# Kernel tuning notes

Hardware: AMD Instinct MI355X
Metric: run time of the kernel (lower is better)

Reference implementation:

```python
import jax, jax.numpy as jnp
import numpy as np

ATTENTION_HEAD = 16
EXPANSION_LENGTH = 300
TEXT_EMBEDDING_DIM = 768
LN_EPS = 1e-3  # keras LayerNormalization default epsilon


def setup_inputs() -> dict:
    key = jax.random.key(0)
    ks = jax.random.split(key, 8)
    B, L, D = 8, 2048, TEXT_EMBEDDING_DIM
    H = ATTENTION_HEAD
    E = EXPANSION_LENGTH
    dh = D // H
    glorot = lambda k, shape, fan_in, fan_out: jax.random.uniform(
        k, shape, jnp.float32,
        -jnp.sqrt(6.0 / (fan_in + fan_out)), jnp.sqrt(6.0 / (fan_in + fan_out)))
    return {
        "q": jax.random.normal(ks[0], (B, 1, L, D), jnp.float32),
        "k": jax.random.normal(ks[1], (B, 1, L, D), jnp.float32),
        "v": jax.random.normal(ks[2], (B, 1, L, D), jnp.float32),
        "Wq": glorot(ks[3], (D, D), D, D),
        "bq": jnp.zeros((D,), jnp.float32),
        "Wv": glorot(ks[4], (D, D), D, D),
        "bv": jnp.zeros((D,), jnp.float32),
        "memory": glorot(ks[5], (E, H, dh), E, dh),
        "gamma": jnp.ones((D,), jnp.float32),
        "beta": jnp.zeros((D,), jnp.float32),
    }


def reference(q, k, v, Wq, bq, Wv, bv, memory, gamma, beta):
    B, _, L, D = q.shape
    H = ATTENTION_HEAD
    dh = D // H
    # Dense projections (v is unused by the original module)
    Q_ = q @ Wq + bq                      # (B,1,L,D)
    V_ = k @ Wv + bv                      # (B,1,L,D)
    Q = Q_.reshape(B, L, H, dh)
    V = V_.reshape(B, L, H, dh)
    # memory-query scores, ReLU instead of softmax
    eij = jax.nn.relu(jnp.einsum('ehd,blhd->belh', memory, Q))  # (B,E,L,H)
    out1 = jnp.einsum('belh,blhd->behd', eij, V)                # (B,E,H,dh)
    out2 = jnp.einsum('behd,belh->blhd', out1, eij)             # (B,L,H,dh)
    x = out2.reshape(B, 1, L, D)
    mean = jnp.mean(x, axis=-1, keepdims=True)
    var = jnp.var(x, axis=-1, keepdims=True)
    return (x - mean) * jax.lax.rsqrt(var + LN_EPS) * gamma + beta
```

## Files before the change

### kernel.cpp

```cpp
#include <hip/hip_runtime.h>
#include <hip/hip_bf16.h>
#include <stdint.h>

#define B_   8
#define L_   2048
#define D_   768
#define H_   16
#define DH   48
#define E_   300
#define EP   320
#define KP   64
#define ACH  8
#define N1T  (128 * DH * EP)
#define NT_  24

typedef __bf16 bf16;
typedef __bf16 bf16x8 __attribute__((ext_vector_type(8)));
typedef __bf16 bf16x4 __attribute__((ext_vector_type(4)));
typedef float  f32x4  __attribute__((ext_vector_type(4)));

typedef const __attribute__((address_space(1))) uint32_t guint;
typedef __attribute__((address_space(3))) uint32_t luint;

__device__ __forceinline__ f32x4 mfma16(bf16x8 a, bf16x8 b, f32x4 c) {
  return __builtin_amdgcn_mfma_f32_16x16x32_bf16(a, b, c, 0, 0, 0);
}

__global__ __launch_bounds__(256) void k_cast(const float* __restrict__ q,
                                              const float* __restrict__ k,
                                              bf16* __restrict__ qc,
                                              bf16* __restrict__ kc) {
  const float* src = blockIdx.y ? k : q;
  bf16* dst = blockIdx.y ? kc : qc;
  const int n8 = B_ * L_ * D_ / 8;
  for (int i = blockIdx.x * 256 + threadIdx.x; i < n8; i += gridDim.x * 256) {
    float4 f0 = *(const float4*)(src + (size_t)i * 8);
    float4 f1 = *(const float4*)(src + (size_t)i * 8 + 4);
    bf16x8 v;
    v[0] = (bf16)f0.x; v[1] = (bf16)f0.y; v[2] = (bf16)f0.z; v[3] = (bf16)f0.w;
    v[4] = (bf16)f1.x; v[5] = (bf16)f1.y; v[6] = (bf16)f1.z; v[7] = (bf16)f1.w;
    *(bf16x8*)(dst + (size_t)i * 8) = v;
  }
}

__global__ __launch_bounds__(256) void k_prep(
    const float* __restrict__ Wq, const float* __restrict__ Wv,
    const float* __restrict__ M, bf16* __restrict__ WqT,
    bf16* __restrict__ WvT, bf16* __restrict__ MP) {
  int bid = blockIdx.x;
  if (bid < 4608) {
    int which = bid / 2304;
    int idx = (bid % 2304) * 256 + threadIdx.x;
    int n = idx / D_, k = idx % D_;
    const float* W = which ? Wv : Wq;
    bf16* WT = which ? WvT : WqT;
    WT[n * D_ + k] = (bf16)W[k * D_ + n];
  } else {
    int idx = (bid - 4608) * 256 + threadIdx.x;
    int h = idx / (EP * KP);
    int r = idx % (EP * KP);
    int e = r / KP, d = r % KP;
    float v = (e < E_ && d < DH) ? M[(e * H_ + h) * DH + d] : 0.f;
    MP[idx] = (bf16)v;
  }
}

__global__ __launch_bounds__(256, 3) void k_gemm(
    const bf16* __restrict__ A0, const bf16* __restrict__ A1,
    const bf16* __restrict__ WT0, const bf16* __restrict__ WT1,
    const float* __restrict__ b0, const float* __restrict__ b1,
    bf16* __restrict__ outQ, bf16* __restrict__ outVT) {
  __shared__ bf16 As[3][128 * 32];
  __shared__ bf16 Bs[3][128 * 32];
  const int tid = threadIdx.x, lane = tid & 63, w = tid >> 6;
  const int wr = w >> 1, wc = w & 1;
  const int lr = lane & 15, lq = lane >> 4;
  const int bid = blockIdx.x;
  const int j = (bid & 7) * 96 + (bid >> 3);
  const int n0 = (j % 6) * 128, m0 = (j / 6) * 128;
  const int mode = blockIdx.y;
  const bf16* A = mode ? A1 : A0;
  const bf16* WT = mode ? WT1 : WT0;
  const float* bias = mode ? b1 : b0;

  auto stage = [&](int buf, int k0) {
#pragma unroll
    for (int p = 0; p < 2; ++p) {
      int idx = tid + p * 256;
      int row = idx >> 2, ct = idx & 3;
      int gc = ct ^ ((row >> 1) & 3);
      const bf16* src = A + (size_t)(m0 + row) * D_ + k0 + gc * 8;
      __builtin_amdgcn_global_load_lds((guint*)src,
          (luint*)&As[buf][(p * 256 + w * 64) * 8], 16, 0, 0);
    }
#pragma unroll
    for (int p = 0; p < 2; ++p) {
      int idx = tid + p * 256;
      int row = idx >> 2, ct = idx & 3;
      int gc = ct ^ ((row >> 1) & 3);
      const bf16* src = WT + (size_t)(n0 + row) * D_ + k0 + gc * 8;
      __builtin_amdgcn_global_load_lds((guint*)src,
          (luint*)&Bs[buf][(p * 256 + w * 64) * 8], 16, 0, 0);
    }
  };

  f32x4 acc[4][4] = {};

  stage(0, 0);
  stage(1, 32);

#pragma unroll
  for (int t = 0; t < NT_; ++t) {
    const int cur = t % 3;
    if (t + 1 < NT_) asm volatile("s_waitcnt vmcnt(4) lgkmcnt(0)" ::: "memory");
    else             asm volatile("s_waitcnt vmcnt(0) lgkmcnt(0)" ::: "memory");
    __builtin_amdgcn_s_barrier();
    __builtin_amdgcn_sched_barrier(0);
    if (t + 2 < NT_) stage((t + 2) % 3, (t + 2) * 32);

    bf16x8 af[4], bfr[4];
#pragma unroll
    for (int mi = 0; mi < 4; ++mi) {
      int row = wr * 64 + mi * 16 + lr;
      af[mi] = *(const bf16x8*)&As[cur][row * 32 + ((lq ^ ((row >> 1) & 3)) * 8)];
    }
#pragma unroll
    for (int ni = 0; ni < 4; ++ni) {
      int row = wc * 64 + ni * 16 + lr;
      bfr[ni] = *(const bf16x8*)&Bs[cur][row * 32 + ((lq ^ ((row >> 1) & 3)) * 8)];
    }
    __builtin_amdgcn_s_setprio(1);
#pragma unroll
    for (int mi = 0; mi < 4; ++mi)
#pragma unroll
      for (int ni = 0; ni < 4; ++ni)
        acc[mi][ni] = mfma16(af[mi], bfr[ni], acc[mi][ni]);
    __builtin_amdgcn_s_setprio(0);
  }

  float bs[4];
#pragma unroll
  for (int ni = 0; ni < 4; ++ni) bs[ni] = bias[n0 + wc * 64 + ni * 16 + lr];

  if (mode == 0) {
#pragma unroll
    for (int mi = 0; mi < 4; ++mi)
#pragma unroll
      for (int ni = 0; ni < 4; ++ni) {
        int m = m0 + wr * 64 + mi * 16 + lq * 4;
        int n = n0 + wc * 64 + ni * 16 + lr;
#pragma unroll
        for (int r = 0; r < 4; ++r)
          outQ[(size_t)(m + r) * D_ + n] = (bf16)(acc[mi][ni][r] + bs[ni]);
      }
  } else {
#pragma unroll
    for (int mi = 0; mi < 4; ++mi)
#pragma unroll
      for (int ni = 0; ni < 4; ++ni) {
        int mb = m0 + wr * 64 + mi * 16 + lq * 4;
        int n = n0 + wc * 64 + ni * 16 + lr;
        int bhd = (mb >> 11) * H_ + n / DH;
        int d = n % DH;
        int l = mb & (L_ - 1);
        bf16x4 v;
#pragma unroll
        for (int r = 0; r < 4; ++r) v[r] = (bf16)(acc[mi][ni][r] + bs[ni]);
        *(bf16x4*)&outVT[((size_t)bhd * DH + d) * L_ + l] = v;
      }
  }
}

__global__ __launch_bounds__(256) void k_phaseA(
    const bf16* __restrict__ Qb, const bf16* __restrict__ VT,
    const bf16* __restrict__ MP, bf16* __restrict__ O1P) {
  __shared__ bf16 Qs[2][32 * 88];
  __shared__ bf16 Vs[2][48 * 40];
  __shared__ bf16 Ss[EP * 40];
  const int tid = threadIdx.x, lane = tid & 63, w = tid >> 6;
  const int lr = lane & 15, lq = lane >> 4;
  const int bid = blockIdx.x;
  const int jj = (bid & 7) * 128 + (bid >> 3);
  const int bh = jj >> 3, b = bh >> 4, h = bh & 15;
  const int ach = jj & 7;
  const int lbase = ach * (L_ / ACH);

  bf16x8 mf[5][2];
#pragma unroll
  for (int mi = 0; mi < 5; ++mi)
#pragma unroll
    for (int kh = 0; kh < 2; ++kh)
      mf[mi][kh] = *(const bf16x8*)&MP[(size_t)(h * EP + w * 80 + mi * 16 + lr) * KP + kh * 32 + lq * 8];

  if (tid < 128) {
    int buf = tid >> 6, t = tid & 63;
    uint4 z = {0, 0, 0, 0};
    *(uint4*)&Qs[buf][(t >> 1) * 88 + 48 + (t & 1) * 8] = z;
  }

  auto loadQ = [&](int idx, int l0) {
    return *(const bf16x8*)&Qb[(size_t)(b * L_ + l0 + idx / 6) * D_ + h * DH + (idx % 6) * 8];
  };
  auto loadV = [&](int j, int l0) {
    return *(const bf16x8*)&VT[((size_t)bh * DH + (j >> 2)) * L_ + l0 + (j & 3) * 8];
  };

  bf16x8 rA, rB;
  {
    int l0 = lbase;
    rA = (tid < 192) ? loadQ(tid, l0) : loadV(tid - 192, l0);
    if (tid < 128) rB = loadV(tid + 64, l0);
  }

  f32x4 acc[5][3] = {};

  for (int it = 0; it < L_ / ACH / 32; ++it) {
    const int cur = it & 1;
    if (tid < 192) *(bf16x8*)&Qs[cur][(tid / 6) * 88 + (tid % 6) * 8] = rA;
    else           *(bf16x8*)&Vs[cur][((tid - 192) >> 2) * 40 + ((tid - 192) & 3) * 8] = rA;
    if (tid < 128) *(bf16x8*)&Vs[cur][((tid + 64) >> 2) * 40 + ((tid + 64) & 3) * 8] = rB;
    __syncthreads();
    if (it + 1 < L_ / ACH / 32) {
      int l0 = lbase + (it + 1) * 32;
      rA = (tid < 192) ? loadQ(tid, l0) : loadV(tid - 192, l0);
      if (tid < 128) rB = loadV(tid + 64, l0);
    }
    bf16x8 qf[2][2];
#pragma unroll
    for (int ni = 0; ni < 2; ++ni)
#pragma unroll
      for (int kh = 0; kh < 2; ++kh)
        qf[ni][kh] = *(const bf16x8*)&Qs[cur][(ni * 16 + lr) * 88 + kh * 32 + lq * 8];
    __builtin_amdgcn_s_setprio(1);
#pragma unroll
    for (int mi = 0; mi < 5; ++mi)
#pragma unroll
      for (int ni = 0; ni < 2; ++ni) {
        f32x4 s = {0.f, 0.f, 0.f, 0.f};
        s = mfma16(mf[mi][0], qf[ni][0], s);
        s = mfma16(mf[mi][1], qf[ni][1], s);
#pragma unroll
        for (int r = 0; r < 4; ++r)
          Ss[(w * 80 + mi * 16 + lq * 4 + r) * 40 + ni * 16 + lr] =
              (bf16)(s[r] > 0.f ? s[r] : 0.f);
      }
    __builtin_amdgcn_s_setprio(0);
    bf16x8 sf[5], vf[3];
#pragma unroll
    for (int mi = 0; mi < 5; ++mi)
      sf[mi] = *(const bf16x8*)&Ss[(w * 80 + mi * 16 + lr) * 40 + lq * 8];
#pragma unroll
    for (int ni = 0; ni < 3; ++ni)
      vf[ni] = *(const bf16x8*)&Vs[cur][(ni * 16 + lr) * 40 + lq * 8];
    __builtin_amdgcn_s_setprio(1);
#pragma unroll
    for (int mi = 0; mi < 5; ++mi)
#pragma unroll
      for (int ni = 0; ni < 3; ++ni)
        acc[mi][ni] = mfma16(sf[mi], vf[ni], acc[mi][ni]);
    __builtin_amdgcn_s_setprio(0);
  }
  bf16* dst = O1P + (size_t)(ach * 128 + bh) * DH * EP;
#pragma unroll
  for (int mi = 0; mi < 5; ++mi)
#pragma unroll
    for (int ni = 0; ni < 3; ++ni) {
      int e = w * 80 + mi * 16 + lq * 4;
      int d = ni * 16 + lr;
      bf16x4 v;
#pragma unroll
      for (int r = 0; r < 4; ++r) v[r] = (bf16)acc[mi][ni][r];
      *(bf16x4*)&dst[(size_t)d * EP + e] = v;
    }
}

__global__ __launch_bounds__(256) void k_red(const bf16* __restrict__ O1P,
                                             bf16* __restrict__ O1T) {
  int i8 = blockIdx.x * 256 + threadIdx.x;
  if (i8 >= N1T / 8) return;
  float s[8] = {};
#pragma unroll
  for (int c = 0; c < ACH; ++c) {
    bf16x8 v = *(const bf16x8*)&O1P[(size_t)c * N1T + (size_t)i8 * 8];
#pragma unroll
    for (int j = 0; j < 8; ++j) s[j] += (float)v[j];
  }
  bf16x8 o;
#pragma unroll
  for (int j = 0; j < 8; ++j) o[j] = (bf16)s[j];
  *(bf16x8*)&O1T[(size_t)i8 * 8] = o;
}

__global__ __launch_bounds__(256, 4) void k_phaseB(
    const bf16* __restrict__ Qb, const bf16* __restrict__ MP,
    const bf16* __restrict__ O1T, bf16* __restrict__ X) {
  __shared__ bf16 Qs[64 * 88];
  __shared__ bf16 STs[64 * 76];
  __shared__ bf16 O1s[2][48 * 76];
  const int tid = threadIdx.x, lane = tid & 63, w = tid >> 6;
  const int lr = lane & 15, lq = lane >> 4;
  const int bid = blockIdx.x;
  const int jj = (bid & 7) * 512 + (bid >> 3);
  const int bh = jj >> 5, b = bh >> 4, h = bh & 15;
  const int l0 = (jj & 31) * 64;

  bf16x8 mfB[5][2];
#pragma unroll
  for (int c = 0; c < 5; ++c)
#pragma unroll
    for (int kh = 0; kh < 2; ++kh)
      mfB[c][kh] = *(const bf16x8*)&MP[(size_t)(h * EP + c * 64 + w * 16 + lr) * KP + kh * 32 + lq * 8];

  for (int idx = tid; idx < 512; idx += 256) {
    if (idx < 384) {
      int row = idx / 6, c = idx % 6;
      *(bf16x8*)&Qs[row * 88 + c * 8] =
          *(const bf16x8*)&Qb[(size_t)(b * L_ + l0 + row) * D_ + h * DH + c * 8];
    } else {
      int j = idx - 384;
      uint4 z = {0, 0, 0, 0};
      *(uint4*)&Qs[(j >> 1) * 88 + 48 + (j & 1) * 8] = z;
    }
  }
  for (int idx = tid; idx < 384; idx += 256)
    *(bf16x8*)&O1s[0][(idx >> 3) * 76 + (idx & 7) * 8] =
        *(const bf16x8*)&O1T[((size_t)bh * DH + (idx >> 3)) * EP + (idx & 7) * 8];
  __syncthreads();

  f32x4 acc[3] = {};
#pragma unroll
  for (int c = 0; c < 5; ++c) {
    bf16x8 r0, r1;
    if (c < 4) {
      r0 = *(const bf16x8*)&O1T[((size_t)bh * DH + (tid >> 3)) * EP + (c + 1) * 64 + (tid & 7) * 8];
      if (tid < 128) {
        int i2 = tid + 256;
        r1 = *(const bf16x8*)&O1T[((size_t)bh * DH + (i2 >> 3)) * EP + (c + 1) * 64 + (i2 & 7) * 8];
      }
    }
    __builtin_amdgcn_s_setprio(1);
#pragma unroll
    for (int mi = 0; mi < 4; ++mi) {
      bf16x8 qa0 = *(const bf16x8*)&Qs[(mi * 16 + lr) * 88 + lq * 8];
      bf16x8 qa1 = *(const bf16x8*)&Qs[(mi * 16 + lr) * 88 + 32 + lq * 8];
      f32x4 s = {0.f, 0.f, 0.f, 0.f};
      s = mfma16(qa0, mfB[c][0], s);
      s = mfma16(qa1, mfB[c][1], s);
#pragma unroll
      for (int r = 0; r < 4; ++r)
        STs[(mi * 16 + lq * 4 + r) * 76 + w * 16 + lr] =
            (bf16)(s[r] > 0.f ? s[r] : 0.f);
    }
    __builtin_amdgcn_s_setprio(0);
    __syncthreads();
    __builtin_amdgcn_s_setprio(1);
#pragma unroll
    for (int ks = 0; ks < 2; ++ks) {
      bf16x8 sf = *(const bf16x8*)&STs[(w * 16 + lr) * 76 + ks * 32 + lq * 8];
#pragma unroll
      for (int ni = 0; ni < 3; ++ni) {
        bf16x8 of = *(const bf16x8*)&O1s[c & 1][(ni * 16 + lr) * 76 + ks * 32 + lq * 8];
        acc[ni] = mfma16(sf, of, acc[ni]);
      }
    }
    __builtin_amdgcn_s_setprio(0);
    if (c < 4) {
      *(bf16x8*)&O1s[(c + 1) & 1][(tid >> 3) * 76 + (tid & 7) * 8] = r0;
      if (tid < 128) {
        int i2 = tid + 256;
        *(bf16x8*)&O1s[(c + 1) & 1][(i2 >> 3) * 76 + (i2 & 7) * 8] = r1;
      }
    }
    __syncthreads();
  }
#pragma unroll
  for (int ni = 0; ni < 3; ++ni)
#pragma unroll
    for (int r = 0; r < 4; ++r)
      X[(size_t)(b * L_ + l0 + w * 16 + lq * 4 + r) * D_ + h * DH + ni * 16 + lr] =
          (bf16)acc[ni][r];
}

__global__ __launch_bounds__(256) void k_ln(
    const bf16* __restrict__ X, const float* __restrict__ gamma,
    const float* __restrict__ beta, float* __restrict__ out) {
  const int lane = threadIdx.x & 63;
  const int row = blockIdx.x * 4 + (threadIdx.x >> 6);
  const bf16* x = X + (size_t)row * D_;
  float v[12];
#pragma unroll
  for (int c = 0; c < 3; ++c) {
    bf16x4 ch = *(const bf16x4*)(x + lane * 12 + c * 4);
#pragma unroll
    for (int j = 0; j < 4; ++j) v[c * 4 + j] = (float)ch[j];
  }
  float s = 0.f, q = 0.f;
#pragma unroll
  for (int j = 0; j < 12; ++j) { s += v[j]; q += v[j] * v[j]; }
#pragma unroll
  for (int off = 32; off > 0; off >>= 1) {
    s += __shfl_xor(s, off);
    q += __shfl_xor(q, off);
  }
  float mean = s * (1.f / 768.f);
  float var = q * (1.f / 768.f) - mean * mean;
  float inv = rsqrtf(var + 1e-3f);
  float* o = out + (size_t)row * D_;
#pragma unroll
  for (int c = 0; c < 3; ++c) {
    float4 g = *(const float4*)(gamma + lane * 12 + c * 4);
    float4 bt = *(const float4*)(beta + lane * 12 + c * 4);
    float4 r;
    r.x = (v[c * 4 + 0] - mean) * inv * g.x + bt.x;
    r.y = (v[c * 4 + 1] - mean) * inv * g.y + bt.y;
    r.z = (v[c * 4 + 2] - mean) * inv * g.z + bt.z;
    r.w = (v[c * 4 + 3] - mean) * inv * g.w + bt.w;
    *(float4*)(o + lane * 12 + c * 4) = r;
  }
}

extern "C" void kernel_launch(void* const* d_in, const int* in_sizes, int n_in,
                              void* d_out, int out_size, void* d_ws, size_t ws_size,
                              hipStream_t stream) {
  (void)in_sizes; (void)n_in; (void)out_size; (void)ws_size;
  const float* q_in = (const float*)d_in[0];
  const float* k_in = (const float*)d_in[1];
  const float* Wq   = (const float*)d_in[3];
  const float* bq   = (const float*)d_in[4];
  const float* Wv   = (const float*)d_in[5];
  const float* bv   = (const float*)d_in[6];
  const float* mem  = (const float*)d_in[7];
  const float* gam  = (const float*)d_in[8];
  const float* bet  = (const float*)d_in[9];
  float* out = (float*)d_out;

  char* ws = (char*)d_ws;
  size_t off = 0;
  auto alloc = [&](size_t bytes) {
    char* p = ws + off;
    off += (bytes + 255) & ~(size_t)255;
    return p;
  };
  bf16*  WqT = (bf16*)alloc((size_t)D_ * D_ * 2);
  bf16*  WvT = (bf16*)alloc((size_t)D_ * D_ * 2);
  bf16*  MP  = (bf16*)alloc((size_t)H_ * EP * KP * 2);
  bf16*  Qb  = (bf16*)alloc((size_t)B_ * L_ * D_ * 2);
  bf16*  VT  = (bf16*)alloc((size_t)B_ * H_ * DH * L_ * 2);
  bf16*  O1T = (bf16*)alloc((size_t)N1T * 2);
  const size_t castHalf  = ((size_t)B_ * L_ * D_ * 2 + 256) & ~(size_t)255;
  const size_t castBytes = 2 * castHalf;
  const size_t o1pBytes  = (size_t)ACH * N1T * 2;
  size_t bigBytes = castBytes > o1pBytes ? castBytes : o1pBytes;
  char*  big = alloc(bigBytes);
  bf16*  qc  = (bf16*)big;
  bf16*  kc  = (bf16*)(big + castHalf);
  bf16*  O1P = (bf16*)big;
  bf16*  Xb  = (bf16*)big;

  k_cast<<<dim3(2048, 2), 256, 0, stream>>>(q_in, k_in, qc, kc);
  k_prep<<<5888, 256, 0, stream>>>(Wq, Wv, mem, WqT, WvT, MP);
  k_gemm<<<dim3(768, 2), 256, 0, stream>>>(qc, kc, WqT, WvT, bq, bv, Qb, VT);
  k_phaseA<<<1024, 256, 0, stream>>>(Qb, VT, MP, O1P);
  k_red<<<(N1T / 8 + 255) / 256, 256, 0, stream>>>(O1P, O1T);
  k_phaseB<<<4096, 256, 0, stream>>>(Qb, MP, O1T, Xb);
  k_ln<<<(B_ * L_) / 4, 256, 0, stream>>>(Xb, gam, bet, out);
}
```

Baseline: 191.9 us.

## Fuse fp32-to-bf16 cast of q/k into GEMM A-tile loading

Removes the separate cast kernel and has the projection GEMM load fp32 activations into registers, convert them to bf16, and write them to swizzled LDS, using a register-staged three-deep prefetch. This drops a full bf16 write and re-read of q and k plus one kernel launch. In exchange, GEMM A-tile traffic doubles (fp32), the loads no longer go directly to LDS, register pressure rises, and the pipeline's wait counts are restructured.

```diff
diff --git a/kernel.cpp b/kernel.cpp
--- a/kernel.cpp
+++ b/kernel.cpp
@@ -24,23 +24,6 @@
 
 __device__ __forceinline__ f32x4 mfma16(bf16x8 a, bf16x8 b, f32x4 c) {
   return __builtin_amdgcn_mfma_f32_16x16x32_bf16(a, b, c, 0, 0, 0);
-}
-
-__global__ __launch_bounds__(256) void k_cast(const float* __restrict__ q,
-                                              const float* __restrict__ k,
-                                              bf16* __restrict__ qc,
-                                              bf16* __restrict__ kc) {
-  const float* src = blockIdx.y ? k : q;
-  bf16* dst = blockIdx.y ? kc : qc;
-  const int n8 = B_ * L_ * D_ / 8;
-  for (int i = blockIdx.x * 256 + threadIdx.x; i < n8; i += gridDim.x * 256) {
-    float4 f0 = *(const float4*)(src + (size_t)i * 8);
-    float4 f1 = *(const float4*)(src + (size_t)i * 8 + 4);
-    bf16x8 v;
-    v[0] = (bf16)f0.x; v[1] = (bf16)f0.y; v[2] = (bf16)f0.z; v[3] = (bf16)f0.w;
-    v[4] = (bf16)f1.x; v[5] = (bf16)f1.y; v[6] = (bf16)f1.z; v[7] = (bf16)f1.w;
-    *(bf16x8*)(dst + (size_t)i * 8) = v;
-  }
 }
 
 __global__ __launch_bounds__(256) void k_prep(
@@ -66,7 +49,7 @@
 }
 
 __global__ __launch_bounds__(256, 3) void k_gemm(
-    const bf16* __restrict__ A0, const bf16* __restrict__ A1,
+    const float* __restrict__ A0, const float* __restrict__ A1,
     const bf16* __restrict__ WT0, const bf16* __restrict__ WT1,
     const float* __restrict__ b0, const float* __restrict__ b1,
     bf16* __restrict__ outQ, bf16* __restrict__ outVT) {
@@ -79,20 +62,15 @@
   const int j = (bid & 7) * 96 + (bid >> 3);
   const int n0 = (j % 6) * 128, m0 = (j / 6) * 128;
   const int mode = blockIdx.y;
-  const bf16* A = mode ? A1 : A0;
+  const float* A = mode ? A1 : A0;
   const bf16* WT = mode ? WT1 : WT0;
   const float* bias = mode ? b1 : b0;
 
-  auto stage = [&](int buf, int k0) {
-#pragma unroll
-    for (int p = 0; p < 2; ++p) {
-      int idx = tid + p * 256;
-      int row = idx >> 2, ct = idx & 3;
-      int gc = ct ^ ((row >> 1) & 3);
-      const bf16* src = A + (size_t)(m0 + row) * D_ + k0 + gc * 8;
-      __builtin_amdgcn_global_load_lds((guint*)src,
-          (luint*)&As[buf][(p * 256 + w * 64) * 8], 16, 0, 0);
-    }
+  const int arow = tid >> 2, ac = tid & 3;
+  const int aslot = ac ^ ((arow >> 1) & 3);
+  const float* aSrc = A + (size_t)(m0 + arow) * D_ + ac * 8;
+
+  auto stageB = [&](int buf, int k0) {
 #pragma unroll
     for (int p = 0; p < 2; ++p) {
       int idx = tid + p * 256;
@@ -105,18 +83,48 @@
   };
 
   f32x4 acc[4][4] = {};
-
-  stage(0, 0);
-  stage(1, 32);
+  float4 ar[3][4];
+
+#define LOADA(G, T)                                                \
+  { const float* s0_ = aSrc + (T) * 32;                            \
+    ar[G][0] = *(const float4*)s0_;                                \
+    ar[G][1] = *(const float4*)(s0_ + 4);                          \
+    const float* s1_ = s0_ + (size_t)64 * D_;                      \
+    ar[G][2] = *(const float4*)s1_;                                \
+    ar[G][3] = *(const float4*)(s1_ + 4); }
+#define COMMITA(G, BUF)                                            \
+  { bf16x8 v_;                                                     \
+    v_[0]=(bf16)ar[G][0].x; v_[1]=(bf16)ar[G][0].y;                \
+    v_[2]=(bf16)ar[G][0].z; v_[3]=(bf16)ar[G][0].w;                \
+    v_[4]=(bf16)ar[G][1].x; v_[5]=(bf16)ar[G][1].y;                \
+    v_[6]=(bf16)ar[G][1].z; v_[7]=(bf16)ar[G][1].w;                \
+    *(bf16x8*)&As[BUF][arow * 32 + aslot * 8] = v_;                \
+    v_[0]=(bf16)ar[G][2].x; v_[1]=(bf16)ar[G][2].y;                \
+    v_[2]=(bf16)ar[G][2].z; v_[3]=(bf16)ar[G][2].w;                \
+    v_[4]=(bf16)ar[G][3].x; v_[5]=(bf16)ar[G][3].y;                \
+    v_[6]=(bf16)ar[G][3].z; v_[7]=(bf16)ar[G][3].w;                \
+    *(bf16x8*)&As[BUF][(arow + 64) * 32 + aslot * 8] = v_; }
+#define SBAR __builtin_amdgcn_sched_barrier(0)
+
+  LOADA(0, 0);  SBAR;
+  stageB(0, 0); SBAR;
+  LOADA(1, 1);  SBAR;
+  stageB(1, 32); SBAR;
+  LOADA(2, 2);  SBAR;
+  COMMITA(0, 0);
 
 #pragma unroll
   for (int t = 0; t < NT_; ++t) {
     const int cur = t % 3;
-    if (t + 1 < NT_) asm volatile("s_waitcnt vmcnt(4) lgkmcnt(0)" ::: "memory");
-    else             asm volatile("s_waitcnt vmcnt(0) lgkmcnt(0)" ::: "memory");
+    if (t + 1 < NT_) { COMMITA((t + 1) % 3, (t + 1) % 3); }
+    else { asm volatile("s_waitcnt vmcnt(0)" ::: "memory"); }
+    asm volatile("s_waitcnt lgkmcnt(0)" ::: "memory");
     __builtin_amdgcn_s_barrier();
-    __builtin_amdgcn_sched_barrier(0);
-    if (t + 2 < NT_) stage((t + 2) % 3, (t + 2) * 32);
+    SBAR;
+    if (t + 2 < NT_) stageB((t + 2) % 3, (t + 2) * 32);
+    SBAR;
+    if (t + 3 < NT_) LOADA(t % 3, t + 3);
+    SBAR;
 
     bf16x8 af[4], bfr[4];
 #pragma unroll
@@ -137,6 +145,9 @@
         acc[mi][ni] = mfma16(af[mi], bfr[ni], acc[mi][ni]);
     __builtin_amdgcn_s_setprio(0);
   }
+#undef LOADA
+#undef COMMITA
+#undef SBAR
 
   float bs[4];
 #pragma unroll
@@ -447,19 +458,14 @@
   bf16*  Qb  = (bf16*)alloc((size_t)B_ * L_ * D_ * 2);
   bf16*  VT  = (bf16*)alloc((size_t)B_ * H_ * DH * L_ * 2);
   bf16*  O1T = (bf16*)alloc((size_t)N1T * 2);
-  const size_t castHalf  = ((size_t)B_ * L_ * D_ * 2 + 256) & ~(size_t)255;
-  const size_t castBytes = 2 * castHalf;
-  const size_t o1pBytes  = (size_t)ACH * N1T * 2;
-  size_t bigBytes = castBytes > o1pBytes ? castBytes : o1pBytes;
-  char*  big = alloc(bigBytes);
-  bf16*  qc  = (bf16*)big;
-  bf16*  kc  = (bf16*)(big + castHalf);
+  const size_t o1pBytes = (size_t)ACH * N1T * 2;
+  const size_t xbBytes  = (size_t)B_ * L_ * D_ * 2;
+  char*  big = alloc(o1pBytes > xbBytes ? o1pBytes : xbBytes);
   bf16*  O1P = (bf16*)big;
   bf16*  Xb  = (bf16*)big;
 
-  k_cast<<<dim3(2048, 2), 256, 0, stream>>>(q_in, k_in, qc, kc);
   k_prep<<<5888, 256, 0, stream>>>(Wq, Wv, mem, WqT, WvT, MP);
-  k_gemm<<<dim3(768, 2), 256, 0, stream>>>(qc, kc, WqT, WvT, bq, bv, Qb, VT);
+  k_gemm<<<dim3(768, 2), 256, 0, stream>>>(q_in, k_in, WqT, WvT, bq, bv, Qb, VT);
   k_phaseA<<<1024, 256, 0, stream>>>(Qb, VT, MP, O1P);
   k_red<<<(N1T / 8 + 255) / 256, 256, 0, stream>>>(O1P, O1T);
   k_phaseB<<<4096, 256, 0, stream>>>(Qb, MP, O1T, Xb);
```

After: 188.0 us. 2.0% less time.

## Merge cast and prep kernels; restructure phaseB to per-wave rows without barriers

Applied to the files above, without the earlier changes.

The separate cast and weight/memory prep kernels are merged into one launch with a flat block index, removing one kernel launch. In phaseB each wave now owns its own 16 rows of Q and computes all 64 score columns itself, so the score tile is written and read only by the same wave and the block-level syncs go away. O1T fragments are read straight from global memory instead of being double-buffered through LDS, and memory fragments are loaded per chunk instead of being kept in registers. This removes barriers and LDS traffic, at the cost of more global/L2 reads and redundant memory-fragment loads across waves.

```diff
diff --git a/kernel.cpp b/kernel.cpp
--- a/kernel.cpp
+++ b/kernel.cpp
@@ -26,37 +26,32 @@
   return __builtin_amdgcn_mfma_f32_16x16x32_bf16(a, b, c, 0, 0, 0);
 }
 
-__global__ __launch_bounds__(256) void k_cast(const float* __restrict__ q,
-                                              const float* __restrict__ k,
-                                              bf16* __restrict__ qc,
-                                              bf16* __restrict__ kc) {
-  const float* src = blockIdx.y ? k : q;
-  bf16* dst = blockIdx.y ? kc : qc;
-  const int n8 = B_ * L_ * D_ / 8;
-  for (int i = blockIdx.x * 256 + threadIdx.x; i < n8; i += gridDim.x * 256) {
+__global__ __launch_bounds__(256) void k_prep2(
+    const float* __restrict__ q, const float* __restrict__ k,
+    const float* __restrict__ Wq, const float* __restrict__ Wv,
+    const float* __restrict__ M, bf16* __restrict__ qc,
+    bf16* __restrict__ kc, bf16* __restrict__ WqT,
+    bf16* __restrict__ WvT, bf16* __restrict__ MP) {
+  int bid = blockIdx.x;
+  if (bid < 12288) {
+    const float* src = bid < 6144 ? q : k;
+    bf16* dst = bid < 6144 ? qc : kc;
+    int i = (bid < 6144 ? bid : bid - 6144) * 256 + threadIdx.x;
     float4 f0 = *(const float4*)(src + (size_t)i * 8);
     float4 f1 = *(const float4*)(src + (size_t)i * 8 + 4);
     bf16x8 v;
     v[0] = (bf16)f0.x; v[1] = (bf16)f0.y; v[2] = (bf16)f0.z; v[3] = (bf16)f0.w;
     v[4] = (bf16)f1.x; v[5] = (bf16)f1.y; v[6] = (bf16)f1.z; v[7] = (bf16)f1.w;
     *(bf16x8*)(dst + (size_t)i * 8) = v;
-  }
-}
-
-__global__ __launch_bounds__(256) void k_prep(
-    const float* __restrict__ Wq, const float* __restrict__ Wv,
-    const float* __restrict__ M, bf16* __restrict__ WqT,
-    bf16* __restrict__ WvT, bf16* __restrict__ MP) {
-  int bid = blockIdx.x;
-  if (bid < 4608) {
-    int which = bid / 2304;
-    int idx = (bid % 2304) * 256 + threadIdx.x;
-    int n = idx / D_, k = idx % D_;
+  } else if (bid < 16896) {
+    int which = (bid - 12288) / 2304;
+    int idx = ((bid - 12288) % 2304) * 256 + threadIdx.x;
+    int n = idx / D_, kk = idx % D_;
     const float* W = which ? Wv : Wq;
     bf16* WT = which ? WvT : WqT;
-    WT[n * D_ + k] = (bf16)W[k * D_ + n];
+    WT[n * D_ + kk] = (bf16)W[kk * D_ + n];
   } else {
-    int idx = (bid - 4608) * 256 + threadIdx.x;
+    int idx = (bid - 16896) * 256 + threadIdx.x;
     int h = idx / (EP * KP);
     int r = idx % (EP * KP);
     int e = r / KP, d = r % KP;
@@ -105,7 +100,6 @@
   };
 
   f32x4 acc[4][4] = {};
-
   stage(0, 0);
   stage(1, 32);
 
@@ -295,21 +289,13 @@
     const bf16* __restrict__ Qb, const bf16* __restrict__ MP,
     const bf16* __restrict__ O1T, bf16* __restrict__ X) {
   __shared__ bf16 Qs[64 * 88];
-  __shared__ bf16 STs[64 * 76];
-  __shared__ bf16 O1s[2][48 * 76];
+  __shared__ bf16 STs[64 * 72];
   const int tid = threadIdx.x, lane = tid & 63, w = tid >> 6;
   const int lr = lane & 15, lq = lane >> 4;
   const int bid = blockIdx.x;
   const int jj = (bid & 7) * 512 + (bid >> 3);
   const int bh = jj >> 5, b = bh >> 4, h = bh & 15;
   const int l0 = (jj & 31) * 64;
-
-  bf16x8 mfB[5][2];
-#pragma unroll
-  for (int c = 0; c < 5; ++c)
-#pragma unroll
-    for (int kh = 0; kh < 2; ++kh)
-      mfB[c][kh] = *(const bf16x8*)&MP[(size_t)(h * EP + c * 64 + w * 16 + lr) * KP + kh * 32 + lq * 8];
 
   for (int idx = tid; idx < 512; idx += 256) {
     if (idx < 384) {
@@ -322,56 +308,42 @@
       *(uint4*)&Qs[(j >> 1) * 88 + 48 + (j & 1) * 8] = z;
     }
   }
-  for (int idx = tid; idx < 384; idx += 256)
-    *(bf16x8*)&O1s[0][(idx >> 3) * 76 + (idx & 7) * 8] =
-        *(const bf16x8*)&O1T[((size_t)bh * DH + (idx >> 3)) * EP + (idx & 7) * 8];
   __syncthreads();
 
+  bf16x8 qa[2];
+  qa[0] = *(const bf16x8*)&Qs[(w * 16 + lr) * 88 + lq * 8];
+  qa[1] = *(const bf16x8*)&Qs[(w * 16 + lr) * 88 + 32 + lq * 8];
+
   f32x4 acc[3] = {};
 #pragma unroll
   for (int c = 0; c < 5; ++c) {
-    bf16x8 r0, r1;
-    if (c < 4) {
-      r0 = *(const bf16x8*)&O1T[((size_t)bh * DH + (tid >> 3)) * EP + (c + 1) * 64 + (tid & 7) * 8];
-      if (tid < 128) {
-        int i2 = tid + 256;
-        r1 = *(const bf16x8*)&O1T[((size_t)bh * DH + (i2 >> 3)) * EP + (c + 1) * 64 + (i2 & 7) * 8];
-      }
-    }
+    bf16x8 mf[4][2];
+#pragma unroll
+    for (int et = 0; et < 4; ++et)
+#pragma unroll
+      for (int kh = 0; kh < 2; ++kh)
+        mf[et][kh] = *(const bf16x8*)&MP[(size_t)(h * EP + c * 64 + et * 16 + lr) * KP + kh * 32 + lq * 8];
     __builtin_amdgcn_s_setprio(1);
 #pragma unroll
-    for (int mi = 0; mi < 4; ++mi) {
-      bf16x8 qa0 = *(const bf16x8*)&Qs[(mi * 16 + lr) * 88 + lq * 8];
-      bf16x8 qa1 = *(const bf16x8*)&Qs[(mi * 16 + lr) * 88 + 32 + lq * 8];
+    for (int et = 0; et < 4; ++et) {
       f32x4 s = {0.f, 0.f, 0.f, 0.f};
-      s = mfma16(qa0, mfB[c][0], s);
-      s = mfma16(qa1, mfB[c][1], s);
+      s = mfma16(qa[0], mf[et][0], s);
+      s = mfma16(qa[1], mf[et][1], s);
 #pragma unroll
       for (int r = 0; r < 4; ++r)
-        STs[(mi * 16 + lq * 4 + r) * 76 + w * 16 + lr] =
+        STs[(w * 16 + lq * 4 + r) * 72 + et * 16 + lr] =
             (bf16)(s[r] > 0.f ? s[r] : 0.f);
     }
     __builtin_amdgcn_s_setprio(0);
-    __syncthreads();
-    __builtin_amdgcn_s_setprio(1);
 #pragma unroll
     for (int ks = 0; ks < 2; ++ks) {
-      bf16x8 sf = *(const bf16x8*)&STs[(w * 16 + lr) * 76 + ks * 32 + lq * 8];
+      bf16x8 sf = *(const bf16x8*)&STs[(w * 16 + lr) * 72 + ks * 32 + lq * 8];
 #pragma unroll
       for (int ni = 0; ni < 3; ++ni) {
-        bf16x8 of = *(const bf16x8*)&O1s[c & 1][(ni * 16 + lr) * 76 + ks * 32 + lq * 8];
+        bf16x8 of = *(const bf16x8*)&O1T[((size_t)bh * DH + ni * 16 + lr) * EP + c * 64 + ks * 32 + lq * 8];
         acc[ni] = mfma16(sf, of, acc[ni]);
       }
     }
-    __builtin_amdgcn_s_setprio(0);
-    if (c < 4) {
-      *(bf16x8*)&O1s[(c + 1) & 1][(tid >> 3) * 76 + (tid & 7) * 8] = r0;
-      if (tid < 128) {
-        int i2 = tid + 256;
-        *(bf16x8*)&O1s[(c + 1) & 1][(i2 >> 3) * 76 + (i2 & 7) * 8] = r1;
-      }
-    }
-    __syncthreads();
   }
 #pragma unroll
   for (int ni = 0; ni < 3; ++ni)
@@ -457,8 +429,7 @@
   bf16*  O1P = (bf16*)big;
   bf16*  Xb  = (bf16*)big;
 
-  k_cast<<<dim3(2048, 2), 256, 0, stream>>>(q_in, k_in, qc, kc);
-  k_prep<<<5888, 256, 0, stream>>>(Wq, Wv, mem, WqT, WvT, MP);
+  k_prep2<<<18176, 256, 0, stream>>>(q_in, k_in, Wq, Wv, mem, qc, kc, WqT, WvT, MP);
   k_gemm<<<dim3(768, 2), 256, 0, stream>>>(qc, kc, WqT, WvT, bq, bv, Qb, VT);
   k_phaseA<<<1024, 256, 0, stream>>>(Qb, VT, MP, O1P);
   k_red<<<(N1T / 8 + 255) / 256, 256, 0, stream>>>(O1P, O1T);
```

Result: slower. 267.9 us (+39.6%).
